# Performance work log

Hardware: AMD Instinct MI355X
Metric: run time of the kernel (lower is better)

## Reference

```python
import jax, jax.numpy as jnp
import numpy as np
import math

N, E, G = 20000, 160000, 256
H, L, R, LAT, TD = 128, 4, 64, 128, 64
CUT = 6.0
NTYPES = 101  # max_atomic_num=100 -> 101 rows, row 0 is padding


def _lin(key, fan_in, fan_out):
    kw, _ = jax.random.split(key)
    w = jax.random.normal(kw, (fan_in, fan_out), jnp.float32) / np.sqrt(fan_in).astype(np.float32)
    b = jnp.zeros((fan_out,), jnp.float32)
    return w, b


def _stack_lin(key, fan_in, fan_out):
    keys = jax.random.split(key, L)
    ws, bs = zip(*[_lin(k, fan_in, fan_out) for k in keys])
    return jnp.stack(ws), jnp.stack(bs)


def setup_inputs() -> dict:
    key = jax.random.key(0)
    ks = list(jax.random.split(key, 24))
    noisy_coords = jax.random.uniform(ks[0], (N, 3), jnp.float32)
    noisy_types = jax.random.randint(ks[1], (N,), 0, NTYPES)
    z = jax.random.normal(ks[2], (G, LAT), jnp.float32)
    t = jax.random.uniform(ks[3], (G,), jnp.float32) * 1000.0
    edge_index = jax.random.randint(ks[4], (2, E), 0, N)
    batch = jnp.sort(jax.random.randint(ks[5], (N,), 0, G))
    lattice = jnp.eye(3, dtype=jnp.float32)[None] * 5.0 + 0.1 * jax.random.normal(ks[6], (G, 3, 3), jnp.float32)
    offsets = jax.random.randint(ks[7], (E, 3), -1, 2).astype(jnp.float32)
    atom_embed = jax.random.normal(ks[8], (NTYPES, H), jnp.float32) * 0.02
    atom_embed = atom_embed.at[0].set(0.0)  # padding_idx=0
    z_w, z_b = _lin(ks[9], LAT, H)
    t_w, t_b = _lin(ks[10], TD, H)
    msg_w1, msg_b1 = _stack_lin(ks[11], H, H)
    msg_w2, msg_b2 = _stack_lin(ks[12], H, 3 * H)
    rbf_w, rbf_b = _stack_lin(ks[13], R, 3 * H)
    U = jax.random.normal(ks[14], (L, H, H), jnp.float32) / np.sqrt(H).astype(np.float32)
    V = jax.random.normal(ks[15], (L, H, H), jnp.float32) / np.sqrt(H).astype(np.float32)
    upd_w1, upd_b1 = _stack_lin(ks[16], 2 * H, H)
    upd_w2, upd_b2 = _stack_lin(ks[17], H, 3 * H)
    hc_w1, hc_b1 = _lin(ks[18], H, H)
    hc_w2, hc_b2 = _lin(ks[19], H, 3)
    ht_w1, ht_b1 = _lin(ks[20], H, H)
    ht_w2, ht_b2 = _lin(ks[21], H, NTYPES)
    return dict(noisy_coords=noisy_coords, noisy_types=noisy_types, z=z, t=t,
                edge_index=edge_index, batch=batch, lattice=lattice, offsets=offsets,
                atom_embed=atom_embed, z_w=z_w, z_b=z_b, t_w=t_w, t_b=t_b,
                msg_w1=msg_w1, msg_b1=msg_b1, msg_w2=msg_w2, msg_b2=msg_b2,
                rbf_w=rbf_w, rbf_b=rbf_b, U=U, V=V,
                upd_w1=upd_w1, upd_b1=upd_b1, upd_w2=upd_w2, upd_b2=upd_b2,
                hc_w1=hc_w1, hc_b1=hc_b1, hc_w2=hc_w2, hc_b2=hc_b2,
                ht_w1=ht_w1, ht_b1=ht_b1, ht_w2=ht_w2, ht_b2=ht_b2)


def reference(noisy_coords, noisy_types, z, t, edge_index, batch, lattice, offsets,
              atom_embed, z_w, z_b, t_w, t_b,
              msg_w1, msg_b1, msg_w2, msg_b2, rbf_w, rbf_b, U, V,
              upd_w1, upd_b1, upd_w2, upd_b2,
              hc_w1, hc_b1, hc_w2, hc_b2, ht_w1, ht_b1, ht_w2, ht_b2):
    n = noisy_coords.shape[0]
    src, dst = edge_index[0], edge_index[1]

    # node embeddings + conditioning
    s = atom_embed[noisy_types]                       # [N, H]
    v = jnp.zeros((n, 3, H), s.dtype)                 # [N, 3, H]
    half = TD // 2
    freqs = jnp.exp(-math.log(10000.0) * jnp.arange(half, dtype=jnp.float32) / (half - 1))
    emb = t[:, None] * freqs[None, :]                 # [G, TD/2]
    t_emb = jnp.concatenate([jnp.sin(emb), jnp.cos(emb)], axis=-1)  # [G, TD]
    cond = (z @ z_w + z_b)[batch] + (t_emb @ t_w + t_b)[batch]      # [N, H]

    # edge geometry: gather -> diff -> 3x3 matmul -> norm -> RBF -> normalize
    frac_diff = noisy_coords[dst] - noisy_coords[src] + offsets     # [E, 3]
    cart = jnp.einsum('ei,eij->ej', frac_diff, lattice[batch[src]]) # [E, 3]
    dist = jnp.maximum(jnp.sqrt(jnp.sum(cart * cart, -1)), 1e-8)    # clamp(min=1e-8)
    centers = jnp.linspace(0.0, CUT, R)
    gamma = jnp.float32(R / CUT)
    rbf = jnp.exp(-gamma * (dist[:, None] - centers[None, :]) ** 2) # [E, R]
    unit = cart / jnp.maximum(jnp.sqrt(jnp.sum(cart * cart, -1, keepdims=True)), 1e-12)

    # PaiNN layers (canonical message + update blocks)
    for l in range(L):
        s = s + cond
        # message block
        phi = jax.nn.silu(s @ msg_w1[l] + msg_b1[l]) @ msg_w2[l] + msg_b2[l]  # [N, 3H]
        filt = rbf @ rbf_w[l] + rbf_b[l]                                      # [E, 3H]
        x = phi[src] * filt
        ds, dv1, dv2 = jnp.split(x, 3, axis=-1)
        s = s + jax.ops.segment_sum(ds, dst, num_segments=n)
        vmsg = dv1[:, None, :] * v[src] + dv2[:, None, :] * unit[:, :, None]  # [E, 3, H]
        v = v + jax.ops.segment_sum(vmsg, dst, num_segments=n)
        # update block
        Uv = jnp.einsum('nch,hk->nck', v, U[l])
        Vv = jnp.einsum('nch,hk->nck', v, V[l])
        Vn = jnp.sqrt(jnp.sum(Vv * Vv, axis=1) + 1e-8)                        # [N, H]
        a = jax.nn.silu(jnp.concatenate([s, Vn], -1) @ upd_w1[l] + upd_b1[l]) @ upd_w2[l] + upd_b2[l]
        avv, asv, ass = jnp.split(a, 3, axis=-1)
        v = v + avv[:, None, :] * Uv
        s = s + asv * jnp.sum(Uv * Vv, axis=1) + ass

    coords_out = jax.nn.silu(s @ hc_w1 + hc_b1) @ hc_w2 + hc_b2   # [N, 3]
    type_out = jax.nn.silu(s @ ht_w1 + ht_b1) @ ht_w2 + ht_b2     # [N, 101]
    return coords_out, type_out
```

## Files before the change

### kernel.cpp

```cpp
#include <hip/hip_runtime.h>
#include <hip/hip_bf16.h>

#define HD 128
#define RD 64
#define H3 384

typedef float f32x4 __attribute__((ext_vector_type(4)));
typedef unsigned short us8 __attribute__((ext_vector_type(8)));
typedef __bf16 bf16x8 __attribute__((ext_vector_type(8)));

__device__ __forceinline__ float silu_f(float x) {
    return x / (1.0f + __expf(-x));
}
__device__ __forceinline__ unsigned short f2bf(float x) {
    __hip_bfloat16 h = __float2bfloat16(x);
    return *reinterpret_cast<unsigned short*>(&h);
}
__device__ __forceinline__ float bf2f(unsigned short u) {
    return __uint_as_float(((unsigned)u) << 16);
}
__device__ __forceinline__ f32x4 mfma3(us8 ah, us8 al, us8 bh, us8 bl, f32x4 c) {
    bf16x8 AH = __builtin_bit_cast(bf16x8, ah);
    bf16x8 AL = __builtin_bit_cast(bf16x8, al);
    bf16x8 BH = __builtin_bit_cast(bf16x8, bh);
    bf16x8 BL = __builtin_bit_cast(bf16x8, bl);
    c = __builtin_amdgcn_mfma_f32_16x16x32_bf16(AH, BH, c, 0, 0, 0);
    c = __builtin_amdgcn_mfma_f32_16x16x32_bf16(AH, BL, c, 0, 0, 0);
    c = __builtin_amdgcn_mfma_f32_16x16x32_bf16(AL, BH, c, 0, 0, 0);
    return c;
}

__global__ void wprep_kernel(const float* __restrict__ src,
                             unsigned short* __restrict__ dhi, unsigned short* __restrict__ dlo,
                             int K, int OUT, int sStride, int dStride, int nlay) {
    int total = K * OUT;
    for (int idx = blockIdx.x * blockDim.x + threadIdx.x; idx < total * nlay;
         idx += gridDim.x * blockDim.x) {
        int lyr = idx / total, r = idx % total;
        int o = r / K, k = r % K;
        float x = src[(size_t)lyr * sStride + (size_t)k * OUT + o];
        unsigned short hi = f2bf(x);
        unsigned short lo = f2bf(x - bf2f(hi));
        dhi[(size_t)lyr * dStride + (size_t)o * K + k] = hi;
        dlo[(size_t)lyr * dStride + (size_t)o * K + k] = lo;
    }
}

__global__ __launch_bounds__(128) void cond_kernel(const float* __restrict__ z, const float* __restrict__ t,
                            const float* __restrict__ z_w, const float* __restrict__ z_b,
                            const float* __restrict__ t_w, const float* __restrict__ t_b,
                            float* __restrict__ condG) {
    int g = blockIdx.x;
    int k = threadIdx.x;
    __shared__ float zr[128];
    __shared__ float te[64];
    zr[k] = z[g * 128 + k];
    if (k < 32) {
        float f = __expf(-9.2103403719761836f * (float)k / 31.0f);
        float e = t[g] * f;
        te[k] = sinf(e);
        te[32 + k] = cosf(e);
    }
    __syncthreads();
    float acc = z_b[k] + t_b[k];
    #pragma unroll 8
    for (int i = 0; i < 128; ++i) acc += zr[i] * z_w[i * 128 + k];
    #pragma unroll 8
    for (int i = 0; i < 64; ++i) acc += te[i] * t_w[i * 128 + k];
    condG[g * 128 + k] = acc;
}

__global__ void init_kernel(const int* __restrict__ types, const float* __restrict__ emb,
                            const float* __restrict__ condG, const int* __restrict__ batch,
                            float* __restrict__ s, int N_) {
    int i = blockIdx.x * blockDim.x + threadIdx.x;
    if (i < N_ * HD) {
        int n = i >> 7;
        int k = i & 127;
        s[i] = emb[types[n] * HD + k] + condG[batch[n] * 128 + k];
    }
}

__global__ void geom_kernel(const float* __restrict__ coords, const int* __restrict__ srcI,
                            const int* __restrict__ dstI, const int* __restrict__ batch,
                            const float* __restrict__ lattice, const float* __restrict__ offs,
                            float* __restrict__ dist, float* __restrict__ unit, int E_) {
    int e = blockIdx.x * blockDim.x + threadIdx.x;
    if (e >= E_) return;
    int sn = srcI[e], dn = dstI[e];
    float f0 = coords[dn * 3 + 0] - coords[sn * 3 + 0] + offs[e * 3 + 0];
    float f1 = coords[dn * 3 + 1] - coords[sn * 3 + 1] + offs[e * 3 + 1];
    float f2 = coords[dn * 3 + 2] - coords[sn * 3 + 2] + offs[e * 3 + 2];
    const float* Lg = lattice + batch[sn] * 9;
    float c0 = f0 * Lg[0] + f1 * Lg[3] + f2 * Lg[6];
    float c1 = f0 * Lg[1] + f1 * Lg[4] + f2 * Lg[7];
    float c2 = f0 * Lg[2] + f1 * Lg[5] + f2 * Lg[8];
    float nrm = sqrtf(c0 * c0 + c1 * c1 + c2 * c2);
    dist[e] = fmaxf(nrm, 1e-8f);
    float inv = 1.0f / fmaxf(nrm, 1e-12f);
    unit[e * 3 + 0] = c0 * inv;
    unit[e * 3 + 1] = c1 * inv;
    unit[e * 3 + 2] = c2 * inv;
}

__global__ void hist_kernel(const int* __restrict__ dstI, int* __restrict__ cnt, int E_) {
    int e = blockIdx.x * blockDim.x + threadIdx.x;
    if (e < E_) atomicAdd(&cnt[dstI[e]], 1);
}

__global__ __launch_bounds__(1024) void scan_kernel(const int* __restrict__ cnt, int* __restrict__ cur, int n) {
    __shared__ int tmp[1024];
    __shared__ int carry_s;
    if (threadIdx.x == 0) carry_s = 0;
    __syncthreads();
    for (int base = 0; base < n; base += 1024) {
        int i = base + threadIdx.x;
        int x = (i < n) ? cnt[i] : 0;
        tmp[threadIdx.x] = x;
        __syncthreads();
        for (int off = 1; off < 1024; off <<= 1) {
            int y = (threadIdx.x >= off) ? tmp[threadIdx.x - off] : 0;
            __syncthreads();
            tmp[threadIdx.x] += y;
            __syncthreads();
        }
        if (i < n) cur[i] = carry_s + tmp[threadIdx.x] - x;
        __syncthreads();
        if (threadIdx.x == 0) carry_s += tmp[1023];
        __syncthreads();
    }
}

__global__ void scatter_kernel(const int* __restrict__ srcI, const int* __restrict__ dstI,
                               const float* __restrict__ dist, const float* __restrict__ unit,
                               int* __restrict__ cur,
                               float* __restrict__ dist_s, float* __restrict__ unit_s,
                               int* __restrict__ src_s, int* __restrict__ dst_s, int E_) {
    int e = blockIdx.x * blockDim.x + threadIdx.x;
    if (e >= E_) return;
    int d = dstI[e];
    int p = atomicAdd(&cur[d], 1);
    dist_s[p] = dist[e];
    unit_s[p * 3 + 0] = unit[e * 3 + 0];
    unit_s[p * 3 + 1] = unit[e * 3 + 1];
    unit_s[p * 3 + 2] = unit[e * 3 + 2];
    src_s[p] = srcI[e];
    dst_s[p] = d;
}

#define PSA 136
__global__ __launch_bounds__(256, 2) void phi_mfma(
    const float* __restrict__ s,
    const unsigned short* __restrict__ w1h, const unsigned short* __restrict__ w1l,
    const float* __restrict__ b1,
    const unsigned short* __restrict__ w2h, const unsigned short* __restrict__ w2l,
    const float* __restrict__ b2,
    float* __restrict__ phi, int N_) {
    __shared__ unsigned short Ah[32 * PSA], Al[32 * PSA], Hh[32 * PSA], Hl[32 * PSA];
    const int tid = threadIdx.x;
    const int n0 = blockIdx.x * 32;
    for (int idx = tid; idx < 32 * 128; idx += 256) {
        int j = idx >> 7, k = idx & 127;
        int n = n0 + j; if (n >= N_) n = N_ - 1;
        float x = s[(size_t)n * 128 + k];
        unsigned short h = f2bf(x);
        Ah[j * PSA + k] = h;
        Al[j * PSA + k] = f2bf(x - bf2f(h));
    }
    __syncthreads();
    const int w = tid >> 6, l = tid & 63;
    const int lr = l & 15, lk = (l >> 4) << 3, rg0 = (l >> 4) << 2;
    const f32x4 zero4 = {0.0f, 0.0f, 0.0f, 0.0f};
    f32x4 acc1[2][2];
    #pragma unroll
    for (int rt = 0; rt < 2; ++rt)
        #pragma unroll
        for (int ci = 0; ci < 2; ++ci) acc1[rt][ci] = zero4;
    #pragma unroll
    for (int kt = 0; kt < 4; ++kt) {
        int kk = kt * 32 + lk;
        us8 bh[2], bl[2], ah[2], alo[2];
        #pragma unroll
        for (int ci = 0; ci < 2; ++ci) {
            int col = (w * 2 + ci) * 16 + lr;
            bh[ci] = *(const us8*)(w1h + (size_t)col * 128 + kk);
            bl[ci] = *(const us8*)(w1l + (size_t)col * 128 + kk);
        }
        #pragma unroll
        for (int rt = 0; rt < 2; ++rt) {
            ah[rt]  = *(const us8*)(Ah + (rt * 16 + lr) * PSA + kk);
            alo[rt] = *(const us8*)(Al + (rt * 16 + lr) * PSA + kk);
        }
        #pragma unroll
        for (int rt = 0; rt < 2; ++rt)
            #pragma unroll
            for (int ci = 0; ci < 2; ++ci)
                acc1[rt][ci] = mfma3(ah[rt], alo[rt], bh[ci], bl[ci], acc1[rt][ci]);
    }
    #pragma unroll
    for (int rt = 0; rt < 2; ++rt)
        #pragma unroll
        for (int ci = 0; ci < 2; ++ci) {
            int col = (w * 2 + ci) * 16 + lr;
            float bb = b1[col];
            #pragma unroll
            for (int rg = 0; rg < 4; ++rg) {
                int j = rt * 16 + rg0 + rg;
                float hv = silu_f(acc1[rt][ci][rg] + bb);
                unsigned short hh = f2bf(hv);
                Hh[j * PSA + col] = hh;
                Hl[j * PSA + col] = f2bf(hv - bf2f(hh));
            }
        }
    __syncthreads();
    f32x4 acc2[2][6];
    #pragma unroll
    for (int rt = 0; rt < 2; ++rt)
        #pragma unroll
        for (int ci = 0; ci < 6; ++ci) acc2[rt][ci] = zero4;
    #pragma unroll
    for (int kt = 0; kt < 4; ++kt) {
        int kk = kt * 32 + lk;
        us8 ah[2], alo[2];
        #pragma unroll
        for (int rt = 0; rt < 2; ++rt) {
            ah[rt]  = *(const us8*)(Hh + (rt * 16 + lr) * PSA + kk);
            alo[rt] = *(const us8*)(Hl + (rt * 16 + lr) * PSA + kk);
        }
        #pragma unroll
        for (int ci = 0; ci < 6; ++ci) {
            int col = (w * 6 + ci) * 16 + lr;
            us8 bh = *(const us8*)(w2h + (size_t)col * 128 + kk);
            us8 bl = *(const us8*)(w2l + (size_t)col * 128 + kk);
            #pragma unroll
            for (int rt = 0; rt < 2; ++rt)
                acc2[rt][ci] = mfma3(ah[rt], alo[rt], bh, bl, acc2[rt][ci]);
        }
    }
    #pragma unroll
    for (int rt = 0; rt < 2; ++rt)
        #pragma unroll
        for (int ci = 0; ci < 6; ++ci) {
            int col = (w * 6 + ci) * 16 + lr;
            float bb = b2[col];
            #pragma unroll
            for (int rg = 0; rg < 4; ++rg) {
                int j = rt * 16 + rg0 + rg;
                int n = n0 + j;
                if (n < N_) phi[(size_t)n * 384 + col] = acc2[rt][ci][rg] + bb;
            }
        }
}

__global__ __launch_bounds__(256, 2) void upd_mfma(
    const unsigned short* __restrict__ Uh, const unsigned short* __restrict__ Ul,
    const unsigned short* __restrict__ Vh, const unsigned short* __restrict__ Vl,
    const unsigned short* __restrict__ w1h, const unsigned short* __restrict__ w1l,
    const float* __restrict__ b1,
    const unsigned short* __restrict__ w2h, const unsigned short* __restrict__ w2l,
    const float* __restrict__ b2,
    float* __restrict__ s, float* __restrict__ v, const float* __restrict__ dv,
    const float* __restrict__ condG, const int* __restrict__ batch, int addcond, int N_) {
    __shared__ unsigned short SMA[2 * 48 * 136];
    __shared__ float UvL[48 * 132];
    __shared__ float VvL[48 * 132];
    unsigned short* VNh = SMA;
    unsigned short* VNl = SMA + 48 * 136;
    unsigned short* A1h = SMA;
    unsigned short* A1l = SMA + 16 * 264;
    unsigned short* a1h = SMA + 32 * 264;
    unsigned short* a1l = SMA + 32 * 264 + 16 * 136;
    float* o384 = VvL;
    const int tid = threadIdx.x;
    const int n0 = blockIdx.x * 16;
    for (int idx = tid; idx < 48 * 128; idx += 256) {
        int r = idx >> 7, k = idx & 127;
        int c = r >> 4, j = r & 15;
        int n = n0 + j; if (n >= N_) n = N_ - 1;
        size_t off = (size_t)n * 384 + c * 128 + k;
        float x = v[off] + dv[off];
        unsigned short h = f2bf(x);
        VNh[r * 136 + k] = h;
        VNl[r * 136 + k] = f2bf(x - bf2f(h));
    }
    __syncthreads();
    const int w = tid >> 6, l = tid & 63;
    const int lr = l & 15, lk = (l >> 4) << 3, rg0 = (l >> 4) << 2;
    const f32x4 zero4 = {0.0f, 0.0f, 0.0f, 0.0f};
    {
        f32x4 acc[3][2];
        #pragma unroll
        for (int rt = 0; rt < 3; ++rt) { acc[rt][0] = zero4; acc[rt][1] = zero4; }
        #pragma unroll
        for (int kt = 0; kt < 4; ++kt) {
            int kk = kt * 32 + lk;
            us8 bh[2], bl[2];
            #pragma unroll
            for (int ci = 0; ci < 2; ++ci) {
                int col = (w * 2 + ci) * 16 + lr;
                bh[ci] = *(const us8*)(Uh + (size_t)col * 128 + kk);
                bl[ci] = *(const us8*)(Ul + (size_t)col * 128 + kk);
            }
            #pragma unroll
            for (int rt = 0; rt < 3; ++rt) {
                us8 ah  = *(const us8*)(VNh + (rt * 16 + lr) * 136 + kk);
                us8 alo = *(const us8*)(VNl + (rt * 16 + lr) * 136 + kk);
                #pragma unroll
                for (int ci = 0; ci < 2; ++ci)
                    acc[rt][ci] = mfma3(ah, alo, bh[ci], bl[ci], acc[rt][ci]);
            }
        }
        #pragma unroll
        for (int rt = 0; rt < 3; ++rt)
            #pragma unroll
            for (int ci = 0; ci < 2; ++ci) {
                int col = (w * 2 + ci) * 16 + lr;
                #pragma unroll
                for (int rg = 0; rg < 4; ++rg)
                    UvL[(rt * 16 + rg0 + rg) * 132 + col] = acc[rt][ci][rg];
            }
        #pragma unroll
        for (int rt = 0; rt < 3; ++rt) { acc[rt][0] = zero4; acc[rt][1] = zero4; }
        #pragma unroll
        for (int kt = 0; kt < 4; ++kt) {
            int kk = kt * 32 + lk;
            us8 bh[2], bl[2];
            #pragma unroll
            for (int ci = 0; ci < 2; ++ci) {
                int col = (w * 2 + ci) * 16 + lr;
                bh[ci] = *(const us8*)(Vh + (size_t)col * 128 + kk);
                bl[ci] = *(const us8*)(Vl + (size_t)col * 128 + kk);
            }
            #pragma unroll
            for (int rt = 0; rt < 3; ++rt) {
                us8 ah  = *(const us8*)(VNh + (rt * 16 + lr) * 136 + kk);
                us8 alo = *(const us8*)(VNl + (rt * 16 + lr) * 136 + kk);
                #pragma unroll
                for (int ci = 0; ci < 2; ++ci)
                    acc[rt][ci] = mfma3(ah, alo, bh[ci], bl[ci], acc[rt][ci]);
            }
        }
        #pragma unroll
        for (int rt = 0; rt < 3; ++rt)
            #pragma unroll
            for (int ci = 0; ci < 2; ++ci) {
                int col = (w * 2 + ci) * 16 + lr;
                #pragma unroll
                for (int rg = 0; rg < 4; ++rg)
                    VvL[(rt * 16 + rg0 + rg) * 132 + col] = acc[rt][ci][rg];
            }
    }
    __syncthreads();
    float dotr[8];
    {
        int k = tid & 127;
        int jb = (tid >> 7) * 8;
        #pragma unroll
        for (int i = 0; i < 8; ++i) {
            int j = jb + i;
            float uv0 = UvL[j * 132 + k], uv1 = UvL[(16 + j) * 132 + k], uv2 = UvL[(32 + j) * 132 + k];
            float vv0 = VvL[j * 132 + k], vv1 = VvL[(16 + j) * 132 + k], vv2 = VvL[(32 + j) * 132 + k];
            dotr[i] = uv0 * vv0 + uv1 * vv1 + uv2 * vv2;
            float vnv = sqrtf(vv0 * vv0 + vv1 * vv1 + vv2 * vv2 + 1e-8f);
            int n = n0 + j; if (n >= N_) n = N_ - 1;
            float sv = s[(size_t)n * 128 + k];
            unsigned short h1 = f2bf(sv);
            A1h[j * 264 + k] = h1;
            A1l[j * 264 + k] = f2bf(sv - bf2f(h1));
            unsigned short h2 = f2bf(vnv);
            A1h[j * 264 + 128 + k] = h2;
            A1l[j * 264 + 128 + k] = f2bf(vnv - bf2f(h2));
        }
    }
    __syncthreads();
    {
        f32x4 acc[2]; acc[0] = zero4; acc[1] = zero4;
        #pragma unroll
        for (int kt = 0; kt < 8; ++kt) {
            int kk = kt * 32 + lk;
            us8 ah  = *(const us8*)(A1h + lr * 264 + kk);
            us8 alo = *(const us8*)(A1l + lr * 264 + kk);
            #pragma unroll
            for (int ci = 0; ci < 2; ++ci) {
                int col = (w * 2 + ci) * 16 + lr;
                us8 bh = *(const us8*)(w1h + (size_t)col * 256 + kk);
                us8 bl = *(const us8*)(w1l + (size_t)col * 256 + kk);
                acc[ci] = mfma3(ah, alo, bh, bl, acc[ci]);
            }
        }
        #pragma unroll
        for (int ci = 0; ci < 2; ++ci) {
            int col = (w * 2 + ci) * 16 + lr;
            float bb = b1[col];
            #pragma unroll
            for (int rg = 0; rg < 4; ++rg) {
                int j = rg0 + rg;
                float hv = silu_f(acc[ci][rg] + bb);
                unsigned short hh = f2bf(hv);
                a1h[j * 136 + col] = hh;
                a1l[j * 136 + col] = f2bf(hv - bf2f(hh));
            }
        }
    }
    __syncthreads();
    {
        f32x4 acc[6];
        #pragma unroll
        for (int ci = 0; ci < 6; ++ci) acc[ci] = zero4;
        #pragma unroll
        for (int kt = 0; kt < 4; ++kt) {
            int kk = kt * 32 + lk;
            us8 ah  = *(const us8*)(a1h + lr * 136 + kk);
            us8 alo = *(const us8*)(a1l + lr * 136 + kk);
            #pragma unroll
            for (int ci = 0; ci < 6; ++ci) {
                int col = (w * 6 + ci) * 16 + lr;
                us8 bh = *(const us8*)(w2h + (size_t)col * 128 + kk);
                us8 bl = *(const us8*)(w2l + (size_t)col * 128 + kk);
                acc[ci] = mfma3(ah, alo, bh, bl, acc[ci]);
            }
        }
        #pragma unroll
        for (int ci = 0; ci < 6; ++ci) {
            int col = (w * 6 + ci) * 16 + lr;
            float bb = b2[col];
            #pragma unroll
            for (int rg = 0; rg < 4; ++rg) {
                int j = rg0 + rg;
                o384[j * 388 + col] = acc[ci][rg] + bb;
            }
        }
    }
    __syncthreads();
    {
        int k = tid & 127;
        int jb = (tid >> 7) * 8;
        #pragma unroll
        for (int i = 0; i < 8; ++i) {
            int j = jb + i;
            int n = n0 + j;
            if (n >= N_) continue;
            float a0  = o384[j * 388 + k];
            float aH  = o384[j * 388 + 128 + k];
            float a2v = o384[j * 388 + 256 + k];
            #pragma unroll
            for (int c = 0; c < 3; ++c) {
                size_t off = (size_t)n * 384 + c * 128 + k;
                v[off] = v[off] + dv[off] + a0 * UvL[(c * 16 + j) * 132 + k];
            }
            float cadd = addcond ? condG[(size_t)batch[n] * 128 + k] : 0.0f;
            s[(size_t)n * 128 + k] += aH * dotr[i] + a2v + cadd;
        }
    }
}

#define EB 64
__global__ __launch_bounds__(256, 2) void edge_mfma(
    const float* __restrict__ phi, const float* __restrict__ v,
    const float* __restrict__ dist_s, const float* __restrict__ unit_s,
    const int* __restrict__ src_s, const int* __restrict__ dst_s,
    const unsigned short* __restrict__ rwh, const unsigned short* __restrict__ rwl,
    const float* __restrict__ rb,
    float* __restrict__ s, float* __restrict__ dv, int E_) {
    __shared__ float filt[16 * 388];
    unsigned short* Rh = (unsigned short*)filt;
    unsigned short* Rl = Rh + 4096;
    const int tid = threadIdx.x;
    const int e0 = blockIdx.x * EB;
    #pragma unroll
    for (int it = 0; it < 16; ++it) {
        int idx = it * 256 + tid;
        int i = idx & 7;
        int l2 = (idx >> 3) & 63;
        int mt = (idx >> 9) & 3;
        int kt = idx >> 11;
        int edge = mt * 16 + (l2 & 15);
        int r = kt * 32 + ((l2 >> 4) << 3) + i;
        float val = 0.0f;
        int ge = e0 + edge;
        if (ge < E_) {
            float d = dist_s[ge];
            float c = 6.0f * (float)r / 63.0f;
            float tt = d - c;
            val = __expf(-(64.0f / 6.0f) * tt * tt);
        }
        unsigned short h = f2bf(val);
        Rh[idx] = h;
        Rl[idx] = f2bf(val - bf2f(h));
    }
    __syncthreads();
    const int w = tid >> 6, l = tid & 63;
    const int lr = l & 15, rg0 = (l >> 4) << 2;
    const f32x4 zero4 = {0.0f, 0.0f, 0.0f, 0.0f};
    f32x4 acc[4][6];
    #pragma unroll
    for (int mt = 0; mt < 4; ++mt)
        #pragma unroll
        for (int nt = 0; nt < 6; ++nt) acc[mt][nt] = zero4;
    #pragma unroll
    for (int kt = 0; kt < 2; ++kt) {
        us8 ah[4], al[4];
        #pragma unroll
        for (int mt = 0; mt < 4; ++mt) {
            int base = ((kt * 4 + mt) * 64 + l) * 8;
            ah[mt] = *(const us8*)(Rh + base);
            al[mt] = *(const us8*)(Rl + base);
        }
        int kk = kt * 32 + ((l >> 4) << 3);
        #pragma unroll
        for (int nt = 0; nt < 6; ++nt) {
            int col = w * 96 + nt * 16 + lr;
            us8 bh = *(const us8*)(rwh + (size_t)col * 64 + kk);
            us8 bl = *(const us8*)(rwl + (size_t)col * 64 + kk);
            #pragma unroll
            for (int mt = 0; mt < 4; ++mt)
                acc[mt][nt] = mfma3(ah[mt], al[mt], bh, bl, acc[mt][nt]);
        }
    }
    const int sub = tid >> 7;
    const int col = tid & 127;
    float b0 = rb[col], b1 = rb[128 + col], b2 = rb[256 + col];
    float as = 0.0f, ad0 = 0.0f, ad1 = 0.0f, ad2 = 0.0f;
    int rd = -1;
    #pragma unroll
    for (int ch = 0; ch < 4; ++ch) {
        __syncthreads();
        #pragma unroll
        for (int nt = 0; nt < 6; ++nt) {
            int c2 = w * 96 + nt * 16 + lr;
            #pragma unroll
            for (int rg = 0; rg < 4; ++rg)
                filt[(rg0 + rg) * 388 + c2] = acc[ch][nt][rg];
        }
        __syncthreads();
        int le0 = ch * 16 + sub * 8;
        for (int i = 0; i < 8; ++i) {
            int e = e0 + le0 + i;
            if (e >= E_) break;
            int dn = dst_s[e];
            if (dn != rd) {
                if (rd >= 0) {
                    atomicAdd(&s[(size_t)rd * 128 + col], as);
                    atomicAdd(&dv[(size_t)rd * 384 + col], ad0);
                    atomicAdd(&dv[(size_t)rd * 384 + 128 + col], ad1);
                    atomicAdd(&dv[(size_t)rd * 384 + 256 + col], ad2);
                }
                as = ad0 = ad1 = ad2 = 0.0f;
                rd = dn;
            }
            int sn = src_s[e];
            int fr = sub * 8 + i;
            float f0 = filt[fr * 388 + col] + b0;
            float f1 = filt[fr * 388 + 128 + col] + b1;
            float f2v = filt[fr * 388 + 256 + col] + b2;
            const float* phr = phi + (size_t)sn * 384;
            const float* vr = v + (size_t)sn * 384;
            float x0 = phr[col] * f0;
            float x1 = phr[128 + col] * f1;
            float x2 = phr[256 + col] * f2v;
            float u0 = unit_s[e * 3 + 0], u1 = unit_s[e * 3 + 1], u2 = unit_s[e * 3 + 2];
            as += x0;
            ad0 += x1 * vr[col] + x2 * u0;
            ad1 += x1 * vr[128 + col] + x2 * u1;
            ad2 += x1 * vr[256 + col] + x2 * u2;
        }
    }
    if (rd >= 0) {
        atomicAdd(&s[(size_t)rd * 128 + col], as);
        atomicAdd(&dv[(size_t)rd * 384 + col], ad0);
        atomicAdd(&dv[(size_t)rd * 384 + 128 + col], ad1);
        atomicAdd(&dv[(size_t)rd * 384 + 256 + col], ad2);
    }
}

#define HPB 8
__global__ __launch_bounds__(128, 4) void heads_kernel(
    const float* __restrict__ s,
    const float* __restrict__ hc_w1, const float* __restrict__ hc_b1,
    const float* __restrict__ hc_w2, const float* __restrict__ hc_b2,
    const float* __restrict__ ht_w1, const float* __restrict__ ht_b1,
    const float* __restrict__ ht_w2, const float* __restrict__ ht_b2,
    float* __restrict__ outc, float* __restrict__ outt, int N_) {
    int n0 = blockIdx.x * HPB;
    int k = threadIdx.x;
    __shared__ float sr[HPB][128];
    __shared__ float h1[HPB][128];
    __shared__ float h2[HPB][128];
    #pragma unroll
    for (int j = 0; j < HPB; ++j) {
        int n = n0 + j;
        sr[j][k] = (n < N_) ? s[(size_t)n * 128 + k] : 0.0f;
    }
    __syncthreads();
    float a[HPB], b[HPB];
    #pragma unroll
    for (int j = 0; j < HPB; ++j) { a[j] = hc_b1[k]; b[j] = ht_b1[k]; }
    for (int h = 0; h < 128; h += 4) {
        float wa0 = hc_w1[h * 128 + k],       wa1 = hc_w1[(h + 1) * 128 + k];
        float wa2 = hc_w1[(h + 2) * 128 + k], wa3 = hc_w1[(h + 3) * 128 + k];
        float wb0 = ht_w1[h * 128 + k],       wb1 = ht_w1[(h + 1) * 128 + k];
        float wb2 = ht_w1[(h + 2) * 128 + k], wb3 = ht_w1[(h + 3) * 128 + k];
        #pragma unroll
        for (int j = 0; j < HPB; ++j) {
            const float4 x = *reinterpret_cast<const float4*>(&sr[j][h]);
            a[j] = fmaf(x.w, wa3, fmaf(x.z, wa2, fmaf(x.y, wa1, fmaf(x.x, wa0, a[j]))));
            b[j] = fmaf(x.w, wb3, fmaf(x.z, wb2, fmaf(x.y, wb1, fmaf(x.x, wb0, b[j]))));
        }
    }
    #pragma unroll
    for (int j = 0; j < HPB; ++j) {
        h1[j][k] = silu_f(a[j]);
        h2[j][k] = silu_f(b[j]);
    }
    __syncthreads();
    if (k < 101) {
        for (int j = 0; j < HPB; ++j) {
            int n = n0 + j;
            if (n >= N_) break;
            float c = ht_b2[k];
            #pragma unroll 4
            for (int h = 0; h < 128; ++h) c += h2[j][h] * ht_w2[h * 101 + k];
            outt[(size_t)n * 101 + k] = c;
        }
    }
    if (k < 3) {
        for (int j = 0; j < HPB; ++j) {
            int n = n0 + j;
            if (n >= N_) break;
            float c = hc_b2[k];
            #pragma unroll 4
            for (int h = 0; h < 128; ++h) c += h1[j][h] * hc_w2[h * 3 + k];
            outc[(size_t)n * 3 + k] = c;
        }
    }
}

extern "C" void kernel_launch(void* const* d_in, const int* in_sizes, int n_in,
                              void* d_out, int out_size, void* d_ws, size_t ws_size,
                              hipStream_t stream) {
    const float* coords  = (const float*)d_in[0];
    const int*   types   = (const int*)d_in[1];
    const float* z       = (const float*)d_in[2];
    const float* t       = (const float*)d_in[3];
    const int*   eidx    = (const int*)d_in[4];
    const int*   batch   = (const int*)d_in[5];
    const float* lattice = (const float*)d_in[6];
    const float* offs    = (const float*)d_in[7];
    const float* aemb    = (const float*)d_in[8];
    const float* z_w     = (const float*)d_in[9];
    const float* z_b     = (const float*)d_in[10];
    const float* t_w     = (const float*)d_in[11];
    const float* t_b     = (const float*)d_in[12];
    const float* msg_w1  = (const float*)d_in[13];
    const float* msg_b1  = (const float*)d_in[14];
    const float* msg_w2  = (const float*)d_in[15];
    const float* msg_b2  = (const float*)d_in[16];
    const float* rbf_w   = (const float*)d_in[17];
    const float* rbf_b   = (const float*)d_in[18];
    const float* Um      = (const float*)d_in[19];
    const float* Vm      = (const float*)d_in[20];
    const float* upd_w1  = (const float*)d_in[21];
    const float* upd_b1  = (const float*)d_in[22];
    const float* upd_w2  = (const float*)d_in[23];
    const float* upd_b2  = (const float*)d_in[24];
    const float* hc_w1   = (const float*)d_in[25];
    const float* hc_b1   = (const float*)d_in[26];
    const float* hc_w2   = (const float*)d_in[27];
    const float* hc_b2   = (const float*)d_in[28];
    const float* ht_w1   = (const float*)d_in[29];
    const float* ht_b1   = (const float*)d_in[30];
    const float* ht_w2   = (const float*)d_in[31];
    const float* ht_b2   = (const float*)d_in[32];

    const int N = in_sizes[1];
    const int G = in_sizes[3];
    const int E = in_sizes[4] / 2;
    const int* srcI = eidx;
    const int* dstI = eidx + E;

    char* ws = (char*)d_ws;
    auto alloc = [&](size_t bytes) {
        char* p = ws;
        ws += (bytes + 255) & ~(size_t)255;
        return p;
    };
    float* s_buf   = (float*)alloc((size_t)N * HD * 4);
    float* v_buf   = (float*)alloc((size_t)N * H3 * 4);
    float* dv_buf  = (float*)alloc((size_t)N * H3 * 4);
    float* phi_buf = (float*)alloc((size_t)N * H3 * 4);
    float* condG   = (float*)alloc((size_t)G * HD * 4);
    float* dist_s  = (float*)alloc((size_t)E * 4);
    float* unit_s  = (float*)alloc((size_t)E * 3 * 4);
    int*   src_s   = (int*)alloc((size_t)E * 4);
    int*   dst_s   = (int*)alloc((size_t)E * 4);
    int*   cur     = (int*)alloc((size_t)N * 4);
    const size_t LS = 409600;
    unsigned short* wpr = (unsigned short*)alloc((size_t)4 * LS * 2);
    float* dist_t  = phi_buf;
    float* unit_t  = phi_buf + E;

    hipMemsetAsync(v_buf, 0, (size_t)N * H3 * 4, stream);
    hipMemsetAsync(cur, 0, (size_t)N * 4, stream);
    cond_kernel<<<G, 128, 0, stream>>>(z, t, z_w, z_b, t_w, t_b, condG);
    init_kernel<<<(N * HD + 255) / 256, 256, 0, stream>>>(types, aemb, condG, batch, s_buf, N);
    geom_kernel<<<(E + 255) / 256, 256, 0, stream>>>(coords, srcI, dstI, batch, lattice, offs, dist_t, unit_t, E);
    hist_kernel<<<(E + 255) / 256, 256, 0, stream>>>(dstI, cur, E);
    {
        int* cnt2 = (int*)(phi_buf + 4 * (size_t)E);
        hipMemcpyAsync(cnt2, cur, (size_t)N * 4, hipMemcpyDeviceToDevice, stream);
        scan_kernel<<<1, 1024, 0, stream>>>(cnt2, cur, N);
    }
    scatter_kernel<<<(E + 255) / 256, 256, 0, stream>>>(srcI, dstI, dist_t, unit_t, cur,
                                                        dist_s, unit_s, src_s, dst_s, E);
    wprep_kernel<<<256, 256, 0, stream>>>(msg_w1, wpr + 0,      wpr + 16384,  128, 128, 16384, (int)LS, 4);
    wprep_kernel<<<768, 256, 0, stream>>>(msg_w2, wpr + 32768,  wpr + 81920,  128, 384, 49152, (int)LS, 4);
    wprep_kernel<<<512, 256, 0, stream>>>(upd_w1, wpr + 131072, wpr + 163840, 256, 128, 32768, (int)LS, 4);
    wprep_kernel<<<768, 256, 0, stream>>>(upd_w2, wpr + 196608, wpr + 245760, 128, 384, 49152, (int)LS, 4);
    wprep_kernel<<<256, 256, 0, stream>>>(Um,     wpr + 294912, wpr + 311296, 128, 128, 16384, (int)LS, 4);
    wprep_kernel<<<256, 256, 0, stream>>>(Vm,     wpr + 327680, wpr + 344064, 128, 128, 16384, (int)LS, 4);
    wprep_kernel<<<384, 256, 0, stream>>>(rbf_w,  wpr + 360448, wpr + 385024, 64,  384, 24576, (int)LS, 4);

    int eblocks = (E + EB - 1) / EB;
    int pblocks = (N + 31) / 32;
    int ublocks = (N + 15) / 16;
    int hblocks = (N + HPB - 1) / HPB;
    for (int l = 0; l < 4; ++l) {
        const unsigned short* L = wpr + (size_t)l * LS;
        phi_mfma<<<pblocks, 256, 0, stream>>>(s_buf,
                L + 0, L + 16384, msg_b1 + (size_t)l * HD,
                L + 32768, L + 81920, msg_b2 + (size_t)l * H3,
                phi_buf, N);
        hipMemsetAsync(dv_buf, 0, (size_t)N * H3 * 4, stream);
        edge_mfma<<<eblocks, 256, 0, stream>>>(phi_buf, v_buf, dist_s, unit_s, src_s, dst_s,
                                               L + 360448, L + 385024,
                                               rbf_b + (size_t)l * H3,
                                               s_buf, dv_buf, E);
        upd_mfma<<<ublocks, 256, 0, stream>>>(
                L + 294912, L + 311296, L + 327680, L + 344064,
                L + 131072, L + 163840, upd_b1 + (size_t)l * HD,
                L + 196608, L + 245760, upd_b2 + (size_t)l * H3,
                s_buf, v_buf, dv_buf, condG, batch, (l < 3) ? 1 : 0, N);
    }
    heads_kernel<<<hblocks, 128, 0, stream>>>(s_buf, hc_w1, hc_b1, hc_w2, hc_b2,
                                        ht_w1, ht_b1, ht_w2, ht_b2,
                                        (float*)d_out, (float*)d_out + (size_t)N * 3, N);
}
```

Measured before the change: 1.620 ms.

## Compute RBF filter per chunk with fewer MFMAs and lower register pressure

```diff
diff --git a/kernel.cpp b/kernel.cpp
--- a/kernel.cpp
+++ b/kernel.cpp
@@ -27,6 +27,14 @@
     c = __builtin_amdgcn_mfma_f32_16x16x32_bf16(AH, BH, c, 0, 0, 0);
     c = __builtin_amdgcn_mfma_f32_16x16x32_bf16(AH, BL, c, 0, 0, 0);
     c = __builtin_amdgcn_mfma_f32_16x16x32_bf16(AL, BH, c, 0, 0, 0);
+    return c;
+}
+__device__ __forceinline__ f32x4 mfma2(us8 ah, us8 bh, us8 bl, f32x4 c) {
+    bf16x8 AH = __builtin_bit_cast(bf16x8, ah);
+    bf16x8 BH = __builtin_bit_cast(bf16x8, bh);
+    bf16x8 BL = __builtin_bit_cast(bf16x8, bl);
+    c = __builtin_amdgcn_mfma_f32_16x16x32_bf16(AH, BH, c, 0, 0, 0);
+    c = __builtin_amdgcn_mfma_f32_16x16x32_bf16(AH, BL, c, 0, 0, 0);
     return c;
 }
 
@@ -455,16 +463,15 @@
 }
 
 #define EB 64
-__global__ __launch_bounds__(256, 2) void edge_mfma(
+__global__ __launch_bounds__(256) void edge_mfma(
     const float* __restrict__ phi, const float* __restrict__ v,
     const float* __restrict__ dist_s, const float* __restrict__ unit_s,
     const int* __restrict__ src_s, const int* __restrict__ dst_s,
     const unsigned short* __restrict__ rwh, const unsigned short* __restrict__ rwl,
     const float* __restrict__ rb,
     float* __restrict__ s, float* __restrict__ dv, int E_) {
+    __shared__ unsigned short Rh[4096];
     __shared__ float filt[16 * 388];
-    unsigned short* Rh = (unsigned short*)filt;
-    unsigned short* Rl = Rh + 4096;
     const int tid = threadIdx.x;
     const int e0 = blockIdx.x * EB;
     #pragma unroll
@@ -484,53 +491,44 @@
             float tt = d - c;
             val = __expf(-(64.0f / 6.0f) * tt * tt);
         }
-        unsigned short h = f2bf(val);
-        Rh[idx] = h;
-        Rl[idx] = f2bf(val - bf2f(h));
-    }
-    __syncthreads();
+        Rh[idx] = f2bf(val);
+    }
     const int w = tid >> 6, l = tid & 63;
     const int lr = l & 15, rg0 = (l >> 4) << 2;
-    const f32x4 zero4 = {0.0f, 0.0f, 0.0f, 0.0f};
-    f32x4 acc[4][6];
-    #pragma unroll
-    for (int mt = 0; mt < 4; ++mt)
-        #pragma unroll
-        for (int nt = 0; nt < 6; ++nt) acc[mt][nt] = zero4;
-    #pragma unroll
-    for (int kt = 0; kt < 2; ++kt) {
-        us8 ah[4], al[4];
-        #pragma unroll
-        for (int mt = 0; mt < 4; ++mt) {
-            int base = ((kt * 4 + mt) * 64 + l) * 8;
-            ah[mt] = *(const us8*)(Rh + base);
-            al[mt] = *(const us8*)(Rl + base);
-        }
-        int kk = kt * 32 + ((l >> 4) << 3);
-        #pragma unroll
-        for (int nt = 0; nt < 6; ++nt) {
-            int col = w * 96 + nt * 16 + lr;
-            us8 bh = *(const us8*)(rwh + (size_t)col * 64 + kk);
-            us8 bl = *(const us8*)(rwl + (size_t)col * 64 + kk);
-            #pragma unroll
-            for (int mt = 0; mt < 4; ++mt)
-                acc[mt][nt] = mfma3(ah[mt], al[mt], bh, bl, acc[mt][nt]);
-        }
-    }
     const int sub = tid >> 7;
     const int col = tid & 127;
-    float b0 = rb[col], b1 = rb[128 + col], b2 = rb[256 + col];
+    float bias[6];
+    #pragma unroll
+    for (int nt = 0; nt < 6; ++nt) bias[nt] = rb[w * 96 + nt * 16 + lr];
+    const f32x4 zero4 = {0.0f, 0.0f, 0.0f, 0.0f};
     float as = 0.0f, ad0 = 0.0f, ad1 = 0.0f, ad2 = 0.0f;
     int rd = -1;
+    __syncthreads();
     #pragma unroll
     for (int ch = 0; ch < 4; ++ch) {
+        f32x4 acc[6];
+        #pragma unroll
+        for (int nt = 0; nt < 6; ++nt) acc[nt] = zero4;
+        #pragma unroll
+        for (int kt = 0; kt < 2; ++kt) {
+            int base = ((kt * 4 + ch) * 64 + l) * 8;
+            us8 ah = *(const us8*)(Rh + base);
+            int kk = kt * 32 + ((l >> 4) << 3);
+            #pragma unroll
+            for (int nt = 0; nt < 6; ++nt) {
+                int c2 = w * 96 + nt * 16 + lr;
+                us8 bh = *(const us8*)(rwh + (size_t)c2 * 64 + kk);
+                us8 bl = *(const us8*)(rwl + (size_t)c2 * 64 + kk);
+                acc[nt] = mfma2(ah, bh, bl, acc[nt]);
+            }
+        }
         __syncthreads();
         #pragma unroll
         for (int nt = 0; nt < 6; ++nt) {
             int c2 = w * 96 + nt * 16 + lr;
             #pragma unroll
             for (int rg = 0; rg < 4; ++rg)
-                filt[(rg0 + rg) * 388 + c2] = acc[ch][nt][rg];
+                filt[(rg0 + rg) * 388 + c2] = acc[nt][rg] + bias[nt];
         }
         __syncthreads();
         int le0 = ch * 16 + sub * 8;
@@ -550,9 +548,9 @@
             }
             int sn = src_s[e];
             int fr = sub * 8 + i;
-            float f0 = filt[fr * 388 + col] + b0;
-            float f1 = filt[fr * 388 + 128 + col] + b1;
-            float f2v = filt[fr * 388 + 256 + col] + b2;
+            float f0 = filt[fr * 388 + col];
+            float f1 = filt[fr * 388 + 128 + col];
+            float f2v = filt[fr * 388 + 256 + col];
             const float* phr = phi + (size_t)sn * 384;
             const float* vr = v + (size_t)sn * 384;
             float x0 = phr[col] * f0;
```

Result: no change. 1.642 ms (+1.3%).
